# Kernel optimization log

Hardware: AMD Instinct MI355X
Metric: run time of the kernel (lower is better)

Reference implementation:

```python
import jax, jax.numpy as jnp
import numpy as np

N = 6144          # active voxels / points
C = 96            # embed_channels
B = 2             # batch size
D = H = W = 32    # sparse spatial shape
K = 16            # PFAS kNN
DEPTH = 4
GRID_OPTS = np.array([[0.1, 0.1, 0.1], [0.4, 0.4, 0.4], [0.2, 0.2, 0.2]], dtype=np.float32)
BN_EPS = 1e-5


def _bn(x, g, b):
    # BatchNorm1d in training mode: batch stats over the point dim, biased var
    m = x.mean(0)
    v = jnp.var(x, axis=0)
    return (x - m) * jax.lax.rsqrt(v + BN_EPS) * g + b


def _seg_sum(x, seg):
    return jax.ops.segment_sum(x, seg, num_segments=N)


def _forward(indices, x, fp_w, fp_b, fp_g, fp_be, att_w1, att_b1, att_w2, att_b2,
             ff_w1, ff_b1, ff_g, ff_be, ff_w2, ff_b2, sa_w1, sa_b1, sa_w2, sa_b2,
             fj_w1, fj_b1, fj_g, fj_be, fj_w2, fj_b2,
             proj_w, proj_g, proj_be, lw_w, lw_g, lw_be, w_w, adp_w,
             fuse_w, fuse_g, fuse_be, conv1_w, bn1_g, bn1_be, conv2_w, bn2_g, bn2_be):
    # ---- CMPFE ----
    p = jax.nn.relu(_bn(x @ fp_w.T + fp_b, fp_g, fp_be))            # [N,9]
    cd, cl, nm = p[:, :3], p[:, 3:6], p[:, 6:9]

    def _att(f, i):
        h = jax.nn.relu(f @ att_w1[i].T + att_b1[i])
        return jax.nn.sigmoid(h @ att_w2[i].T + att_b2[i])

    enh = jnp.concatenate([cd, cl * _att(cl, 0), nm * _att(nm, 1)], axis=1)
    fu = jax.nn.relu(_bn(enh @ ff_w1.T + ff_b1, ff_g, ff_be)) @ ff_w2.T + ff_b2
    sem = jax.nn.sigmoid(jax.nn.relu(fu @ sa_w1.T + sa_b1) @ sa_w2.T + sa_b2)
    feat = fu * sem + x * (1.0 - sem)                               # new x.features

    # ---- PFAS: kNN geometry stats ----
    coord = indices[:, 1:].astype(jnp.float32)                      # [N,3]
    batch = indices[:, 0]
    sq = jnp.sum(coord * coord, axis=1)
    d2 = sq[:, None] + sq[None, :] - 2.0 * (coord @ coord.T)
    dist = jnp.sqrt(jnp.maximum(d2, 1e-12))
    same = batch[None, :] == batch[:, None]
    eye = jnp.eye(N, dtype=bool)
    dist = jnp.where(same & ~eye, dist, jnp.inf)
    neg_nd, idx = jax.lax.top_k(-dist, K)                           # K nearest
    nbr = coord[idx]                                                # [N,K,3]
    cent = nbr - nbr.mean(axis=1, keepdims=True)
    cov = jnp.einsum('nkd,nke->nde', cent, cent) / (K - 1)
    S = jnp.linalg.svd(cov, compute_uv=False)                       # [N,3] descending
    Sn = S / (S.sum(axis=1, keepdims=True) + 1e-6)
    linearity = Sn[:, 0:1] - (Sn[:, 1] + Sn[:, 2])[:, None]
    mean_dist = (-neg_nd).mean(axis=1, keepdims=True)
    density = 1.0 / (mean_dist + 1e-6)
    fl = jax.nn.relu(_bn(feat @ fj_w1.T + fj_b1, fj_g, fj_be)) @ fj_w2.T + fj_b2
    fp_ = jax.nn.softmax(fl, axis=1)
    tower = (density * 2.0 + fp_[:, 0:1]) / 3.0
    backg = (jnp.maximum(1.0 - linearity, 1.0 - density) + fp_[:, 1:2]) / 3.0
    line = (linearity * 2.0 + fp_[:, 2:3]) / 3.0
    go = jnp.asarray(GRID_OPTS)
    lg = go[2] * jnp.array([1.0, 1.0, 5.0], jnp.float32)            # last dim *5
    grid_sizes = tower * go[0] + backg * go[1] + line * lg + 1e-6   # [N,3]

    # ---- representative grids (N > 200 path) ----
    gm = grid_sizes.mean(axis=1)
    order = jnp.argsort(gm)
    reps = [grid_sizes[order[100:200]].mean(0),
            grid_sizes[order[::-1][:100]].mean(0),
            grid_sizes[order[:100]].mean(0)]

    # ---- voxel-grid clustering (torch_geometric voxel_grid + unique inverse) ----
    start = coord.min(axis=0)

    def _cluster(size):
        size = jnp.clip(size, 1e-6, None)
        c = jnp.clip(jnp.floor((coord - start) / size).astype(jnp.int64), 0, 4095)
        mx = c.max(axis=0) + 1
        ids = ((batch.astype(jnp.int64) * mx[0] + c[:, 0]) * mx[1] + c[:, 1]) * mx[2] + c[:, 2]
        _, inv = jnp.unique(ids, return_inverse=True, size=N, fill_value=0)
        return inv.reshape(-1)

    # ---- adaptive multi-branch scatter softmax aggregation ----
    branch_feats = []
    for i in range(DEPTH - 1):
        seg = _cluster(reps[i])
        cnt = jnp.maximum(_seg_sum(jnp.ones((N, 1), feat.dtype), seg), 1.0)
        pw = jax.nn.relu(_bn(feat @ lw_w[i].T, lw_g[i], lw_be[i]))
        pw = pw - (_seg_sum(pw, seg) / cnt)[seg]
        pw = pw @ w_w[i].T
        pw = jnp.exp(pw - pw.max())
        pw = pw / (_seg_sum(pw, seg)[seg] + 1e-6)
        pf = jax.nn.relu(_bn(feat @ proj_w[i].T, proj_g[i], proj_be[i])) * pw
        branch_feats.append(_seg_sum(pf, seg)[seg])
    adp = jax.nn.softmax(feat @ adp_w.T, axis=1)                    # [N,3]
    agg = jnp.einsum('nc,ncd->nd', adp, jnp.stack(branch_feats, 1))
    last = jax.nn.relu(_bn(feat @ proj_w[-1].T, proj_g[-1], proj_be[-1]))
    fused = jax.nn.relu(_bn(jnp.concatenate([last, agg], 1) @ fuse_w.T, fuse_g, fuse_be)) + feat
    res = fused

    # ---- submanifold sparse conv block (dense scatter form; inactive sites zero,
    #      outputs gathered only at active sites == SubMConv3d) ----
    bi, zi, yi, xi = indices[:, 0], indices[:, 1], indices[:, 2], indices[:, 3]

    def _subm(f, w):
        grid = jnp.zeros((B, D, H, W, C), f.dtype).at[bi, zi, yi, xi].set(f)
        o = jax.lax.conv_general_dilated(grid, w, (1, 1, 1), 'SAME',
                                         dimension_numbers=('NDHWC', 'DHWIO', 'NDHWC'))
        return o[bi, zi, yi, xi]

    f1 = jax.nn.relu(_bn(_subm(fused, conv1_w), bn1_g, bn1_be))
    f2 = _bn(_subm(f1, conv2_w), bn2_g, bn2_be)
    return jax.nn.relu(f2 + res)


def setup_inputs() -> dict:
    key = jax.random.key(0)
    ks = iter(jax.random.split(key, 64))

    def rn(*shape, s=0.05):
        return jax.random.normal(next(ks), shape, jnp.float32) * s

    # unique active voxel coordinates
    rng = np.random.default_rng(0)
    flat = rng.choice(B * D * H * W, size=N, replace=False)
    b = flat // (D * H * W)
    r = flat % (D * H * W)
    z = r // (H * W)
    y = (r % (H * W)) // W
    xw = r % W
    indices = jnp.asarray(np.stack([b, z, y, xw], 1).astype(np.int32))
    Ch = C // 2
    return {
        'x': jax.random.normal(next(ks), (N, C), jnp.float32),
        'indices': indices,
        'fp_w': rn(9, C), 'fp_b': rn(9), 'fp_g': jnp.ones(9), 'fp_be': jnp.zeros(9),
        'att_w1': rn(2, 16, 3), 'att_b1': rn(2, 16), 'att_w2': rn(2, 3, 16), 'att_b2': rn(2, 3),
        'ff_w1': rn(C, 9), 'ff_b1': rn(C), 'ff_g': jnp.ones(C), 'ff_be': jnp.zeros(C),
        'ff_w2': rn(C, C), 'ff_b2': rn(C),
        'sa_w1': rn(Ch, C), 'sa_b1': rn(Ch), 'sa_w2': rn(1, Ch), 'sa_b2': rn(1),
        'fj_w1': rn(64, C), 'fj_b1': rn(64), 'fj_g': jnp.ones(64), 'fj_be': jnp.zeros(64),
        'fj_w2': rn(3, 64), 'fj_b2': rn(3),
        'proj_w': rn(DEPTH, C, C), 'proj_g': jnp.ones((DEPTH, C)), 'proj_be': jnp.zeros((DEPTH, C)),
        'lw_w': rn(DEPTH - 1, C, C), 'lw_g': jnp.ones((DEPTH - 1, C)), 'lw_be': jnp.zeros((DEPTH - 1, C)),
        'w_w': rn(DEPTH - 1, C, C),
        'adp_w': rn(DEPTH - 1, C),
        'fuse_w': rn(C, 2 * C), 'fuse_g': jnp.ones(C), 'fuse_be': jnp.zeros(C),
        'conv1_w': rn(3, 3, 3, C, C), 'bn1_g': jnp.ones(C), 'bn1_be': jnp.zeros(C),
        'conv2_w': rn(3, 3, 3, C, C), 'bn2_g': jnp.ones(C), 'bn2_be': jnp.zeros(C),
    }


def reference(x, indices, fp_w, fp_b, fp_g, fp_be, att_w1, att_b1, att_w2, att_b2,
              ff_w1, ff_b1, ff_g, ff_be, ff_w2, ff_b2, sa_w1, sa_b1, sa_w2, sa_b2,
              fj_w1, fj_b1, fj_g, fj_be, fj_w2, fj_b2,
              proj_w, proj_g, proj_be, lw_w, lw_g, lw_be, w_w, adp_w,
              fuse_w, fuse_g, fuse_be, conv1_w, bn1_g, bn1_be, conv2_w, bn2_g, bn2_be):
    return _forward(indices, x, fp_w, fp_b, fp_g, fp_be, att_w1, att_b1, att_w2, att_b2,
                    ff_w1, ff_b1, ff_g, ff_be, ff_w2, ff_b2, sa_w1, sa_b1, sa_w2, sa_b2,
                    fj_w1, fj_b1, fj_g, fj_be, fj_w2, fj_b2,
                    proj_w, proj_g, proj_be, lw_w, lw_g, lw_be, w_w, adp_w,
                    fuse_w, fuse_g, fuse_be, conv1_w, bn1_g, bn1_be, conv2_w, bn2_g, bn2_be)
```

## Files before the change

### kernel.cpp

```cpp
#include <hip/hip_runtime.h>
#include <cstdint>

#define NPTS 6144
#define CH 96
#define NCELEM (NPTS*CH)
#define HTSZ 16384

__device__ __forceinline__ unsigned fenc(float f){
  unsigned u = __float_as_uint(f);
  return (u & 0x80000000u) ? ~u : (u | 0x80000000u);
}
__device__ __forceinline__ float fdec(unsigned u){
  unsigned b = (u & 0x80000000u) ? (u & 0x7FFFFFFFu) : ~u;
  return __uint_as_float(b);
}

__device__ void eig3(double a00,double a01,double a02,double a11,double a12,double a22,
                     double &e0,double &e1,double &e2){
  double p1 = a01*a01 + a02*a02 + a12*a12;
  double q = (a00+a11+a22)/3.0;
  double b00=a00-q, b11=a11-q, b22=a22-q;
  double p2 = b00*b00 + b11*b11 + b22*b22 + 2.0*p1;
  if (p2 <= 1e-300){ e0=e1=e2=q; return; }
  double pp = sqrt(p2/6.0);
  double inv = 1.0/pp;
  double c00=b00*inv, c01=a01*inv, c02=a02*inv, c11=b11*inv, c12=a12*inv, c22=b22*inv;
  double det = c00*(c11*c22-c12*c12) - c01*(c01*c22-c12*c02) + c02*(c01*c12-c11*c02);
  double r = det*0.5;
  r = r < -1.0 ? -1.0 : (r > 1.0 ? 1.0 : r);
  double phi = acos(r)/3.0;
  e0 = q + 2.0*pp*cos(phi);
  e2 = q + 2.0*pp*cos(phi + 2.0943951023931953);
  e1 = 3.0*q - e0 - e2;
}

__global__ void k_zero(int* p, long n){
  long i = (long)blockIdx.x*blockDim.x + threadIdx.x;
  long st = (long)gridDim.x*blockDim.x;
  for (; i < n; i += st) p[i] = 0;
}
__global__ void k_init(int* table, int* startmin){
  int i = blockIdx.x*blockDim.x + threadIdx.x;
  if (i < 2*32*32*32) table[i] = -1;
  if (i < 3) startmin[i] = 0x7fffffff;
}
__global__ void k_htinit(unsigned long long* keys, int* vals){
  int i = blockIdx.x*blockDim.x + threadIdx.x;
  if (i < 3*HTSZ){ keys[i] = ~0ull; vals[i] = 0x7fffffff; }
}
__global__ void k_pack_min(const int* __restrict__ ind, unsigned* __restrict__ packed, int* startmin){
  __shared__ int mn[3];
  if (threadIdx.x < 3) mn[threadIdx.x] = 0x7fffffff;
  __syncthreads();
  int p = blockIdx.x*blockDim.x + threadIdx.x;
  if (p < NPTS){
    int b = ind[p*4], z = ind[p*4+1], y = ind[p*4+2], x = ind[p*4+3];
    packed[p] = (unsigned)((b<<15)|(z<<10)|(y<<5)|x);
    atomicMin(&mn[0], z); atomicMin(&mn[1], y); atomicMin(&mn[2], x);
  }
  __syncthreads();
  if (threadIdx.x < 3) atomicMin(&startmin[threadIdx.x], mn[threadIdx.x]);
}

__global__ void __launch_bounds__(256) k_mm(
    const float* __restrict__ Abase, const float* __restrict__ Wbase,
    const float* __restrict__ biasBase, float* __restrict__ Obase,
    int CIN, int COUT,
    long sA, long sW, long sO, long sBias,
    const float* __restrict__ statsBase, long sStats,
    const float* __restrict__ gBase, const float* __restrict__ beBase, long sGB,
    const float* __restrict__ SsumBase, const int* __restrict__ segBase, const int* __restrict__ cntBase,
    unsigned* maxenc, int mode)
{
  int zb = blockIdx.y;
  const float* A = Abase + (long)zb*sA;
  const float* W = Wbase + (long)zb*sW;
  float* O = Obase + (long)zb*sO;
  const float* st = statsBase ? statsBase + (long)zb*sStats : nullptr;
  const float* g  = gBase ? gBase + (long)zb*sGB : nullptr;
  const float* be = beBase ? beBase + (long)zb*sGB : nullptr;
  const float* Ss = SsumBase ? SsumBase + (long)zb*NCELEM : nullptr;
  const int* seg  = segBase ? segBase + (long)zb*NPTS : nullptr;
  const int* cnt  = cntBase ? cntBase + (long)zb*NPTS : nullptr;

  __shared__ float Al[32*97];
  __shared__ float Wl[96*97];
  int tid = threadIdx.x;
  int r0 = blockIdx.x*32;
  for (int idx = tid; idx < CIN*COUT; idx += 256){
    int co = idx / CIN, k = idx - co*CIN;
    Wl[k*97 + co] = W[idx];
  }
  for (int idx = tid; idx < 32*CIN; idx += 256){
    int ir = idx / CIN, k = idx - ir*CIN;
    int row = r0 + ir;
    float v = A[(long)row*CIN + k];
    if (mode >= 1) v = fmaxf((v - st[k*2])*st[k*2+1]*g[k] + be[k], 0.f);
    if (mode == 2){
      int s = seg[row];
      float cf = fmaxf((float)cnt[s], 1.f);
      v -= Ss[(long)s*CH + k] / cf;
    }
    Al[ir*97 + k] = v;
  }
  __syncthreads();
  float lmax = -3.4e38f;
  if (COUT == 96){
    int rp = tid >> 4, cg = tid & 15;
    int co0 = cg*6;
    float acc0[6], acc1[6];
    #pragma unroll
    for (int j=0;j<6;++j){
      float b = biasBase ? biasBase[(long)zb*sBias + co0 + j] : 0.f;
      acc0[j] = b; acc1[j] = b;
    }
    int ra = 2*rp, rb = ra+1;
    for (int k=0;k<CIN;++k){
      float a0 = Al[ra*97+k], a1 = Al[rb*97+k];
      #pragma unroll
      for (int j=0;j<6;++j){
        float w = Wl[k*97+co0+j];
        acc0[j] = fmaf(a0, w, acc0[j]);
        acc1[j] = fmaf(a1, w, acc1[j]);
      }
    }
    #pragma unroll
    for (int j=0;j<6;++j){
      O[(long)(r0+ra)*96 + co0 + j] = acc0[j];
      O[(long)(r0+rb)*96 + co0 + j] = acc1[j];
      lmax = fmaxf(lmax, fmaxf(acc0[j], acc1[j]));
    }
  } else {
    for (int idx = tid; idx < 32*COUT; idx += 256){
      int ir = idx/COUT, co = idx - ir*COUT;
      float acc = biasBase ? biasBase[(long)zb*sBias + co] : 0.f;
      for (int k=0;k<CIN;++k) acc = fmaf(Al[ir*97+k], Wl[k*97+co], acc);
      O[(long)(r0+ir)*COUT + co] = acc;
      lmax = fmaxf(lmax, acc);
    }
  }
  if (maxenc){
    __shared__ float rmx[256];
    rmx[tid] = lmax; __syncthreads();
    for (int s2=128; s2>0; s2>>=1){
      if (tid < s2) rmx[tid] = fmaxf(rmx[tid], rmx[tid+s2]);
      __syncthreads();
    }
    if (tid == 0) atomicMax(&maxenc[zb], fenc(rmx[0]));
  }
}

__global__ void __launch_bounds__(256) k_mm_fuse(
    const float* __restrict__ tp3, const float* __restrict__ st,
    const float* __restrict__ pg3, const float* __restrict__ pbe3,
    const float* __restrict__ agg, const float* __restrict__ fw, float* __restrict__ tf)
{
  __shared__ float Al[32*193];
  __shared__ float Wl[96*97];
  int tid = threadIdx.x, r0 = blockIdx.x*32;
  for (int idx = tid; idx < 32*192; idx += 256){
    int ir = idx/192, k = idx - ir*192;
    int row = r0 + ir;
    float v;
    if (k < 96){
      v = tp3[(long)row*96 + k];
      v = fmaxf((v - st[k*2])*st[k*2+1]*pg3[k] + pbe3[k], 0.f);
    } else {
      v = agg[(long)row*96 + (k-96)];
    }
    Al[ir*193 + k] = v;
  }
  int rp = tid >> 4, cg = tid & 15, co0 = cg*6;
  float acc0[6] = {0,0,0,0,0,0}, acc1[6] = {0,0,0,0,0,0};
  int ra = 2*rp, rb = ra+1;
  for (int h=0; h<2; ++h){
    __syncthreads();
    for (int idx = tid; idx < 96*96; idx += 256){
      int co = idx/96, k = idx - co*96;
      Wl[k*97+co] = fw[(long)co*192 + h*96 + k];
    }
    __syncthreads();
    for (int k=0;k<96;++k){
      float a0 = Al[ra*193 + h*96 + k], a1 = Al[rb*193 + h*96 + k];
      #pragma unroll
      for (int j=0;j<6;++j){
        float w = Wl[k*97+co0+j];
        acc0[j] = fmaf(a0, w, acc0[j]);
        acc1[j] = fmaf(a1, w, acc1[j]);
      }
    }
  }
  #pragma unroll
  for (int j=0;j<6;++j){
    tf[(long)(r0+ra)*96 + co0 + j] = acc0[j];
    tf[(long)(r0+rb)*96 + co0 + j] = acc1[j];
  }
}

__global__ void k_stats(const float* __restrict__ Abase, long sA, int COLS,
                        float* __restrict__ statsBase, long sStats){
  int col = blockIdx.x, zb = blockIdx.y;
  const float* A = Abase + (long)zb*sA;
  double s = 0.0, q = 0.0;
  for (int r = threadIdx.x; r < NPTS; r += 256){
    double v = (double)A[(long)r*COLS + col];
    s += v; q += v*v;
  }
  __shared__ double ls[256], lq[256];
  ls[threadIdx.x] = s; lq[threadIdx.x] = q; __syncthreads();
  for (int t=128; t>0; t>>=1){
    if (threadIdx.x < t){ ls[threadIdx.x] += ls[threadIdx.x+t]; lq[threadIdx.x] += lq[threadIdx.x+t]; }
    __syncthreads();
  }
  if (threadIdx.x == 0){
    double mean = ls[0]/NPTS;
    double var = lq[0]/NPTS - mean*mean;
    float* stp = statsBase + (long)zb*sStats + col*2;
    stp[0] = (float)mean;
    stp[1] = (float)(1.0/sqrt(var + 1e-5));
  }
}

__global__ void k_p_att_enh(const float* __restrict__ t9, const float* __restrict__ st,
                            const float* __restrict__ fg, const float* __restrict__ fbe,
                            const float* __restrict__ aw1, const float* __restrict__ ab1,
                            const float* __restrict__ aw2, const float* __restrict__ ab2,
                            float* __restrict__ enh){
  int p = blockIdx.x*blockDim.x + threadIdx.x;
  if (p >= NPTS) return;
  float pp[9];
  #pragma unroll
  for (int c=0;c<9;++c){
    float v = t9[p*9+c];
    pp[c] = fmaxf((v - st[c*2])*st[c*2+1]*fg[c] + fbe[c], 0.f);
  }
  float eo[9];
  eo[0]=pp[0]; eo[1]=pp[1]; eo[2]=pp[2];
  #pragma unroll
  for (int i=0;i<2;++i){
    const float* w1 = aw1 + i*48;
    const float* b1 = ab1 + i*16;
    const float* w2 = aw2 + i*48;
    const float* b2 = ab2 + i*3;
    const float* f = pp + 3 + i*3;
    float h[16];
    #pragma unroll
    for (int j=0;j<16;++j){
      float s = b1[j];
      #pragma unroll
      for (int k=0;k<3;++k) s = fmaf(f[k], w1[j*3+k], s);
      h[j] = fmaxf(s, 0.f);
    }
    #pragma unroll
    for (int o=0;o<3;++o){
      float s = b2[o];
      #pragma unroll
      for (int j=0;j<16;++j) s = fmaf(h[j], w2[o*16+j], s);
      float a = 1.f/(1.f + expf(-s));
      eo[3+i*3+o] = f[o]*a;
    }
  }
  #pragma unroll
  for (int c=0;c<9;++c) enh[p*9+c] = eo[c];
}

__global__ void __launch_bounds__(256) k_sem_feat(
    const float* __restrict__ fu, const float* __restrict__ x,
    const float* __restrict__ w1, const float* __restrict__ b1,
    const float* __restrict__ w2, const float* __restrict__ b2,
    float* __restrict__ feat){
  int wid = (blockIdx.x*blockDim.x + threadIdx.x) >> 6;
  int lane = threadIdx.x & 63;
  if (wid >= NPTS) return;
  const float* fr = fu + (long)wid*96;
  float partial = 0.f;
  if (lane < 48){
    float h = b1[lane];
    for (int k=0;k<96;++k) h = fmaf(fr[k], w1[lane*96+k], h);
    h = fmaxf(h, 0.f);
    partial = h * w2[lane];
  }
  for (int m=32; m; m>>=1) partial += __shfl_xor(partial, m);
  float sem = 1.f/(1.f + expf(-(partial + b2[0])));
  for (int c=lane; c<96; c+=64){
    float f = fr[c];
    feat[(long)wid*96+c] = f*sem + x[(long)wid*96+c]*(1.f - sem);
  }
}

__global__ void __launch_bounds__(256) k_knn(const unsigned* __restrict__ packed,
                                             const int* __restrict__ table,
                                             float* __restrict__ density, float* __restrict__ linearity){
  __shared__ unsigned pk[NPTS];
  for (int i=threadIdx.x; i<NPTS; i+=256) pk[i] = packed[i];
  __syncthreads();
  int pid = blockIdx.x*4 + (threadIdx.x>>6);
  int lane = threadIdx.x & 63;
  unsigned mypc = pk[pid];
  int myb = (int)(mypc>>15);
  int mz = (int)((mypc>>10)&31), my_=(int)((mypc>>5)&31), mx_=(int)(mypc&31);
  unsigned s[16];
  #pragma unroll
  for (int t=0;t<16;++t) s[t] = 0xFFFFFFFFu;
  int cnt = 0;
  const int tbase = myb*32768;
  for (int it=0; it<21; ++it){
    int i = lane + it*64;
    if (i < 1331){
      int dz = i/121;
      int rm = i - dz*121;
      int dy = rm/11;
      int dx = rm - dy*11;
      dz -= 5; dy -= 5; dx -= 5;
      int d2 = dz*dz + dy*dy + dx*dx;
      int zz = mz+dz, yy = my_+dy, xx = mx_+dx;
      if (d2 > 0 && d2 <= 25 &&
          (unsigned)zz < 32u && (unsigned)yy < 32u && (unsigned)xx < 32u){
        int j = table[tbase + (zz*32+yy)*32+xx];
        if (j >= 0){
          ++cnt;
          unsigned key = ((unsigned)d2<<13) | (unsigned)j;
          if (key < s[15]){
            s[15] = key;
            #pragma unroll
            for (int t=15;t>0;--t){
              unsigned a = s[t-1], b = s[t];
              unsigned lo = a<b?a:b, hi = a<b?b:a;
              s[t-1]=lo; s[t]=hi;
            }
          }
        }
      }
    }
  }
  for (int m=32; m; m>>=1) cnt += __shfl_xor(cnt, m);
  if (cnt < 16){
    #pragma unroll
    for (int t=0;t<16;++t) s[t] = 0xFFFFFFFFu;
    for (int it=0; it<96; ++it){
      int j = lane + it*64;
      unsigned pc = pk[j];
      if (j != pid && (int)(pc>>15) == myb){
        int dz = (int)((pc>>10)&31) - mz;
        int dy = (int)((pc>>5)&31) - my_;
        int dx = (int)(pc&31) - mx_;
        unsigned d2 = (unsigned)(dz*dz + dy*dy + dx*dx);
        unsigned key = (d2<<13) | (unsigned)j;
        if (key < s[15]){
          s[15] = key;
          #pragma unroll
          for (int t=15;t>0;--t){
            unsigned a = s[t-1], b = s[t];
            unsigned lo = a<b?a:b, hi = a<b?b:a;
            s[t-1]=lo; s[t]=hi;
          }
        }
      }
    }
  }
  float sdist = 0.f;
  int sz=0,sy=0,sx=0,szz=0,syy=0,sxx=0,szy=0,szx=0,syx=0;
  for (int r=0;r<16;++r){
    unsigned m = s[0];
    #pragma unroll
    for (int w=32; w; w>>=1){
      unsigned o = (unsigned)__shfl_xor((int)m, w);
      m = m<o ? m : o;
    }
    bool own = (s[0] == m);
    #pragma unroll
    for (int t=0;t<15;++t) s[t] = own ? s[t+1] : s[t];
    if (own) s[15] = 0xFFFFFFFFu;
    unsigned idx = m & 8191u;
    unsigned d2 = m >> 13;
    sdist += sqrtf((float)d2);
    unsigned pc = pk[idx];
    int nz=(int)((pc>>10)&31), ny=(int)((pc>>5)&31), nx=(int)(pc&31);
    sz+=nz; sy+=ny; sx+=nx;
    szz+=nz*nz; syy+=ny*ny; sxx+=nx*nx; szy+=nz*ny; szx+=nz*nx; syx+=ny*nx;
  }
  if (lane == 0){
    double m0 = sz/16.0, m1 = sy/16.0, m2 = sx/16.0;
    float c00 = (float)(((double)szz - 16.0*m0*m0)/15.0);
    float c11 = (float)(((double)syy - 16.0*m1*m1)/15.0);
    float c22 = (float)(((double)sxx - 16.0*m2*m2)/15.0);
    float c01 = (float)(((double)szy - 16.0*m0*m1)/15.0);
    float c02 = (float)(((double)szx - 16.0*m0*m2)/15.0);
    float c12 = (float)(((double)syx - 16.0*m1*m2)/15.0);
    double e0,e1,e2;
    eig3((double)c00,(double)c01,(double)c02,(double)c11,(double)c12,(double)c22, e0,e1,e2);
    float s0 = (float)fabs(e0), s1 = (float)fabs(e1), s2 = (float)fabs(e2);
    float den = s0 + s1 + s2 + 1e-6f;
    float sn0 = s0/den, sn1 = s1/den, sn2 = s2/den;
    linearity[pid] = sn0 - (sn1 + sn2);
    float md = sdist * (1.f/16.f);
    density[pid] = 1.f/(md + 1e-6f);
  }
}

__global__ void k_geo(const float* __restrict__ t64, const float* __restrict__ st,
                      const float* __restrict__ fg, const float* __restrict__ fbe,
                      const float* __restrict__ w2, const float* __restrict__ b2,
                      const float* __restrict__ density, const float* __restrict__ linearity,
                      float* __restrict__ gsz, float* __restrict__ gm){
  int p = blockIdx.x*blockDim.x + threadIdx.x;
  if (p >= NPTS) return;
  float fl[3];
  #pragma unroll
  for (int o=0;o<3;++o) fl[o] = b2[o];
  for (int k=0;k<64;++k){
    float v = t64[(long)p*64+k];
    v = fmaxf((v - st[k*2])*st[k*2+1]*fg[k] + fbe[k], 0.f);
    #pragma unroll
    for (int o=0;o<3;++o) fl[o] = fmaf(v, w2[o*64+k], fl[o]);
  }
  float mx = fmaxf(fl[0], fmaxf(fl[1], fl[2]));
  float e0 = expf(fl[0]-mx), e1 = expf(fl[1]-mx), e2 = expf(fl[2]-mx);
  float es = e0+e1+e2;
  float p0 = e0/es, p1 = e1/es, p2 = e2/es;
  float den = density[p], lin = linearity[p];
  float tw = (den*2.f + p0)/3.f;
  float bg = (fmaxf(1.f-lin, 1.f-den) + p1)/3.f;
  float ln = (lin*2.f + p2)/3.f;
  float g0 = tw*0.1f + bg*0.4f + ln*0.2f + 1e-6f;
  float g1 = tw*0.1f + bg*0.4f + ln*0.2f + 1e-6f;
  float g2 = tw*0.1f + bg*0.4f + ln*1.0f + 1e-6f;
  gsz[p*3+0]=g0; gsz[p*3+1]=g1; gsz[p*3+2]=g2;
  gm[p] = (g0+g1+g2)/3.f;
}

#define RNKCHUNK 768
__global__ void __launch_bounds__(256) k_rank(const float* __restrict__ gm, int* __restrict__ rank){
  __shared__ unsigned long long lk[RNKCHUNK];
  int j0 = blockIdx.y*RNKCHUNK;
  for (int i=threadIdx.x; i<RNKCHUNK; i+=256){
    int j = j0 + i;
    lk[i] = (((unsigned long long)fenc(gm[j]))<<13) | (unsigned long long)j;
  }
  __syncthreads();
  int p = blockIdx.x*256 + threadIdx.x;
  unsigned long long myk = (((unsigned long long)fenc(gm[p]))<<13) | (unsigned long long)p;
  int cnt = 0;
  #pragma unroll 4
  for (int i=0; i<RNKCHUNK; ++i) cnt += (lk[i] < myk) ? 1 : 0;
  atomicAdd(&rank[p], cnt);
}
__global__ void k_scatter(const int* __restrict__ rank, const float* __restrict__ gsz,
                          float* __restrict__ bkt){
  int p = blockIdx.x*blockDim.x + threadIdx.x;
  if (p >= NPTS) return;
  int r = rank[p];
  int z = -1, t = 0;
  if (r < 100){ z = 2; t = r; }
  else if (r < 200){ z = 0; t = r - 100; }
  else if (r >= NPTS-100){ z = 1; t = r - (NPTS-100); }
  if (z >= 0){
    #pragma unroll
    for (int d=0; d<3; ++d) bkt[(z*100 + t)*3 + d] = gsz[p*3+d];
  }
}
__global__ void k_reps(const float* __restrict__ bkt, float* __restrict__ reps){
  int i = threadIdx.x;
  if (i >= 9) return;
  int z = i/3, d = i - z*3;
  double s = 0.0;
  for (int t=0; t<100; ++t) s += (double)bkt[(z*100 + t)*3 + d];
  reps[i] = (float)(s/100.0);
}

__global__ void k_cluster_c(const int* __restrict__ ind, const float* __restrict__ reps,
                            const int* __restrict__ startmin, int* __restrict__ cbuf, int* mxbuf){
  int z = blockIdx.y;
  int p = blockIdx.x*blockDim.x + threadIdx.x;
  __shared__ int lmx[3];
  if (threadIdx.x < 3) lmx[threadIdx.x] = 0;
  __syncthreads();
  if (p < NPTS){
    #pragma unroll
    for (int d=0; d<3; ++d){
      float sizev = fmaxf(reps[z*3+d], 1e-6f);
      float cf = floorf(((float)ind[p*4+1+d] - (float)startmin[d]) / sizev);
      int ci = (int)cf;
      ci = ci < 0 ? 0 : (ci > 4095 ? 4095 : ci);
      cbuf[((long)z*NPTS + p)*3 + d] = ci;
      atomicMax(&lmx[d], ci);
    }
  }
  __syncthreads();
  if (threadIdx.x < 3) atomicMax(&mxbuf[z*3+threadIdx.x], lmx[threadIdx.x]);
// ... 223 lines not shown
}
__global__ void __launch_bounds__(256) k_conv_sum(const int* __restrict__ nbrtab,
                                                  const float* __restrict__ part,
                                                  float* __restrict__ out){
  int idx = blockIdx.x*256 + threadIdx.x;
  int p = idx/24, c4 = idx - p*24;
  const int* nt = nbrtab + p*27;
  float4 acc = make_float4(0.f,0.f,0.f,0.f);
  for (int tap=0; tap<27; ++tap){
    if (nt[tap] >= 0){
      float4 v = ((const float4*)part)[((long)p*27 + tap)*24 + c4];
      acc.x += v.x; acc.y += v.y; acc.z += v.z; acc.w += v.w;
    }
  }
  ((float4*)out)[idx] = acc;
}
__global__ void __launch_bounds__(256) k_conv_gemm_atomic(
    const float* __restrict__ src, const float* __restrict__ Wc,
    const int* __restrict__ tapcnt, const int* __restrict__ ptlist,
    float* __restrict__ out){
  int tap = blockIdx.y;
  int n = tapcnt[tap];
  int r0 = blockIdx.x*32;
  if (r0 >= n) return;
  __shared__ float Al[32*97];
  __shared__ float Wl[96*97];
  __shared__ int pqs[32];
  int tid = threadIdx.x;
  if (tid < 32){
    int r = r0 + tid;
    pqs[tid] = (r < n) ? ptlist[tap*NPTS + r] : -1;
  }
  __syncthreads();
  for (int idx4 = tid; idx4 < 2304; idx4 += 256){
    int ci = idx4/24, c4 = idx4 - ci*24;
    float4 w = ((const float4*)(Wc + ((long)tap*96 + ci)*96))[c4];
    float* d = &Wl[ci*97 + c4*4];
    d[0]=w.x; d[1]=w.y; d[2]=w.z; d[3]=w.w;
  }
  for (int idx4 = tid; idx4 < 32*24; idx4 += 256){
    int ir = idx4/24, c4 = idx4 - ir*24;
    int pq = pqs[ir];
    float4 s = make_float4(0.f,0.f,0.f,0.f);
    if (pq >= 0){
      int q = pq & 0xFFFF;
      s = ((const float4*)(src + (long)q*CH))[c4];
    }
    float* d = &Al[ir*97 + c4*4];
    d[0]=s.x; d[1]=s.y; d[2]=s.z; d[3]=s.w;
  }
  __syncthreads();
  int rp = tid >> 4, cg = tid & 15;
  int co0 = cg*6;
  int ra = 2*rp, rb = ra+1;
  float acc0[6]={0,0,0,0,0,0}, acc1[6]={0,0,0,0,0,0};
  for (int k=0;k<96;++k){
    float a0 = Al[ra*97+k], a1 = Al[rb*97+k];
    #pragma unroll
    for (int j=0;j<6;++j){
      float w = Wl[k*97+co0+j];
      acc0[j] = fmaf(a0, w, acc0[j]);
      acc1[j] = fmaf(a1, w, acc1[j]);
    }
  }
  int pa = pqs[ra], pb = pqs[rb];
  if (pa >= 0){
    float* o = out + (long)(pa>>16)*CH + co0;
    #pragma unroll
    for (int j=0;j<6;++j) atomicAdd(&o[j], acc0[j]);
  }
  if (pb >= 0){
    float* o = out + (long)(pb>>16)*CH + co0;
    #pragma unroll
    for (int j=0;j<6;++j) atomicAdd(&o[j], acc1[j]);
  }
}
__global__ void k_bnrelu(const float* __restrict__ a, const float* __restrict__ st,
                         const float* __restrict__ g, const float* __restrict__ be,
                         float* __restrict__ o){
  int idx = blockIdx.x*blockDim.x + threadIdx.x;
  int c = idx % CH;
  float v = a[idx];
  o[idx] = fmaxf((v - st[c*2])*st[c*2+1]*g[c] + be[c], 0.f);
}
__global__ void k_final(const float* __restrict__ c2, const float* __restrict__ st,
                        const float* __restrict__ g, const float* __restrict__ be,
                        const float* __restrict__ fused, float* __restrict__ out){
  int idx = blockIdx.x*blockDim.x + threadIdx.x;
  int c = idx % CH;
  float v = c2[idx];
  v = (v - st[c*2])*st[c*2+1]*g[c] + be[c];
  out[idx] = fmaxf(v + fused[idx], 0.f);
}

extern "C" void kernel_launch(void* const* d_in, const int* in_sizes, int n_in,
                              void* d_out, int out_size, void* d_ws, size_t ws_size,
                              hipStream_t stream)
{
  const float* x      = (const float*)d_in[0];
  const int*   ind    = (const int*)  d_in[1];
  const float* fp_w   = (const float*)d_in[2];
  const float* fp_b   = (const float*)d_in[3];
  const float* fp_g   = (const float*)d_in[4];
  const float* fp_be  = (const float*)d_in[5];
  const float* att_w1 = (const float*)d_in[6];
  const float* att_b1 = (const float*)d_in[7];
  const float* att_w2 = (const float*)d_in[8];
  const float* att_b2 = (const float*)d_in[9];
  const float* ff_w1  = (const float*)d_in[10];
  const float* ff_b1  = (const float*)d_in[11];
  const float* ff_g   = (const float*)d_in[12];
  const float* ff_be  = (const float*)d_in[13];
  const float* ff_w2  = (const float*)d_in[14];
  const float* ff_b2  = (const float*)d_in[15];
  const float* sa_w1  = (const float*)d_in[16];
  const float* sa_b1  = (const float*)d_in[17];
  const float* sa_w2  = (const float*)d_in[18];
  const float* sa_b2  = (const float*)d_in[19];
  const float* fj_w1  = (const float*)d_in[20];
  const float* fj_b1  = (const float*)d_in[21];
  const float* fj_g   = (const float*)d_in[22];
  const float* fj_be  = (const float*)d_in[23];
  const float* fj_w2  = (const float*)d_in[24];
  const float* fj_b2  = (const float*)d_in[25];
  const float* proj_w = (const float*)d_in[26];
  const float* proj_g = (const float*)d_in[27];
  const float* proj_be= (const float*)d_in[28];
  const float* lw_w   = (const float*)d_in[29];
  const float* lw_g   = (const float*)d_in[30];
  const float* lw_be  = (const float*)d_in[31];
  const float* w_w    = (const float*)d_in[32];
  const float* adp_w  = (const float*)d_in[33];
  const float* fuse_w = (const float*)d_in[34];
  const float* fuse_g = (const float*)d_in[35];
  const float* fuse_be= (const float*)d_in[36];
  const float* conv1_w= (const float*)d_in[37];
  const float* bn1_g  = (const float*)d_in[38];
  const float* bn1_be = (const float*)d_in[39];
  const float* conv2_w= (const float*)d_in[40];
  const float* bn2_g  = (const float*)d_in[41];
  const float* bn2_be = (const float*)d_in[42];
  float* outp = (float*)d_out;
  (void)in_sizes; (void)n_in; (void)out_size;

  char* ws = (char*)d_ws;
  size_t off = 0;
  auto alloc = [&](size_t bytes)->size_t{
    off = (off + 255) & ~(size_t)255;
    size_t o = off; off += bytes; return o;
  };
  const size_t FNC = (size_t)NCELEM*4;
  size_t o_packed = alloc((size_t)NPTS*4);
  size_t o_start  = alloc(16);
  size_t o_dens   = alloc((size_t)NPTS*4);
  size_t o_lin    = alloc((size_t)NPTS*4);
  size_t o_t9     = alloc((size_t)NPTS*9*4);
  size_t o_enh    = alloc((size_t)NPTS*9*4);
  size_t o_gm     = alloc((size_t)NPTS*4);
  size_t o_gsz    = alloc((size_t)NPTS*3*4);
  size_t o_reps   = alloc(16*4);
  size_t o_bkt    = alloc((size_t)3*100*3*4);
  size_t o_cbuf   = alloc((size_t)3*NPTS*3*4);
  size_t o_ids    = alloc((size_t)3*NPTS*8);
  size_t o_seg    = alloc((size_t)3*NPTS*4);
  size_t o_adp    = alloc((size_t)NPTS*3*4);
  size_t o_table  = alloc((size_t)65536*4);
  size_t o_nbr    = alloc((size_t)NPTS*27*4);
  size_t o_ptlist = alloc((size_t)27*NPTS*4);
  size_t o_t64    = alloc((size_t)NPTS*64*4);
  size_t o_stats  = alloc((size_t)13*192*4);
  size_t o_htk    = alloc((size_t)3*HTSZ*8);
  size_t o_htv    = alloc((size_t)3*HTSZ*4);
  size_t o_S      = alloc(3*FNC);
  size_t o_E      = alloc(3*FNC);
  size_t o_F      = alloc(3*FNC);
  size_t o_cnt    = alloc((size_t)3*NPTS*4);
  size_t o_rank   = alloc((size_t)NPTS*4);
  size_t o_tapcnt = alloc(32*4);
  size_t o_mx     = alloc(16*4);
  size_t o_maxenc = alloc(16*4);
  size_t zend = off;
  size_t o_T96 = alloc(FNC);
  size_t o_fu  = alloc(FNC);
  size_t o_feat= alloc(FNC);
  size_t o_tlw = alloc(3*FNC);
  size_t o_pw2 = alloc(3*FNC);
  size_t o_tp  = alloc(4*FNC);
  size_t o_agg = alloc(FNC);
  size_t o_tf  = alloc(FNC);
  size_t o_fsd = alloc(FNC);
  size_t o_c1  = alloc(FNC);
  size_t o_f1  = alloc(FNC);
  size_t o_c2  = alloc(FNC);
  size_t need_base = off;
  size_t o_part = alloc((size_t)NPTS*27*CH*4);
  bool use_part = (off <= ws_size);
  (void)need_base;

  float* stats = (float*)(ws + o_stats);
  long zcount = (long)((zend - o_S)/4);

  k_zero<<<dim3(2048), dim3(256), 0, stream>>>((int*)(ws+o_S), zcount);
  k_init<<<dim3(256), dim3(256), 0, stream>>>((int*)(ws+o_table), (int*)(ws+o_start));
  k_htinit<<<dim3((3*HTSZ+255)/256), dim3(256), 0, stream>>>((unsigned long long*)(ws+o_htk), (int*)(ws+o_htv));
  k_pack_min<<<dim3(24), dim3(256), 0, stream>>>(ind, (unsigned*)(ws+o_packed), (int*)(ws+o_start));
  k_table<<<dim3(24), 256, 0, stream>>>(ind, (int*)(ws+o_table));

  k_mm<<<dim3(192,1), 256, 0, stream>>>(x, fp_w, fp_b, (float*)(ws+o_t9), 96, 9,
      0,0,0,0, nullptr,0, nullptr,nullptr,0, nullptr,nullptr,nullptr, nullptr, 0);
  k_stats<<<dim3(9,1), 256, 0, stream>>>((float*)(ws+o_t9), 0, 9, stats+0*192, 0);
  k_p_att_enh<<<dim3(24), 256, 0, stream>>>((float*)(ws+o_t9), stats+0*192, fp_g, fp_be,
      att_w1, att_b1, att_w2, att_b2, (float*)(ws+o_enh));

  k_mm<<<dim3(192,1), 256, 0, stream>>>((float*)(ws+o_enh), ff_w1, ff_b1, (float*)(ws+o_T96), 9, 96,
      0,0,0,0, nullptr,0, nullptr,nullptr,0, nullptr,nullptr,nullptr, nullptr, 0);
  k_stats<<<dim3(96,1), 256, 0, stream>>>((float*)(ws+o_T96), 0, 96, stats+1*192, 0);
  k_mm<<<dim3(192,1), 256, 0, stream>>>((float*)(ws+o_T96), ff_w2, ff_b2, (float*)(ws+o_fu), 96, 96,
      0,0,0,0, stats+1*192,0, ff_g, ff_be,0, nullptr,nullptr,nullptr, nullptr, 1);

  k_sem_feat<<<dim3(1536), 256, 0, stream>>>((float*)(ws+o_fu), x, sa_w1, sa_b1, sa_w2, sa_b2,
      (float*)(ws+o_feat));

  k_knn<<<dim3(1536), 256, 0, stream>>>((unsigned*)(ws+o_packed), (int*)(ws+o_table),
      (float*)(ws+o_dens), (float*)(ws+o_lin));

  k_mm<<<dim3(192,1), 256, 0, stream>>>((float*)(ws+o_feat), fj_w1, fj_b1, (float*)(ws+o_t64), 96, 64,
      0,0,0,0, nullptr,0, nullptr,nullptr,0, nullptr,nullptr,nullptr, nullptr, 0);
  k_stats<<<dim3(64,1), 256, 0, stream>>>((float*)(ws+o_t64), 0, 64, stats+2*192, 0);
  k_geo<<<dim3(24), 256, 0, stream>>>((float*)(ws+o_t64), stats+2*192, fj_g, fj_be, fj_w2, fj_b2,
      (float*)(ws+o_dens), (float*)(ws+o_lin), (float*)(ws+o_gsz), (float*)(ws+o_gm));

  k_rank<<<dim3(24,8), 256, 0, stream>>>((float*)(ws+o_gm), (int*)(ws+o_rank));
  k_scatter<<<dim3(24), 256, 0, stream>>>((int*)(ws+o_rank), (float*)(ws+o_gsz), (float*)(ws+o_bkt));
  k_reps<<<dim3(1), 64, 0, stream>>>((float*)(ws+o_bkt), (float*)(ws+o_reps));

  k_cluster_c<<<dim3(24,3), 256, 0, stream>>>(ind, (float*)(ws+o_reps), (int*)(ws+o_start),
      (int*)(ws+o_cbuf), (int*)(ws+o_mx));
  k_cluster_ids<<<dim3(24,3), 256, 0, stream>>>(ind, (int*)(ws+o_cbuf), (int*)(ws+o_mx),
      (long long*)(ws+o_ids));
  k_seg_build<<<dim3(24,3), 256, 0, stream>>>((long long*)(ws+o_ids),
      (unsigned long long*)(ws+o_htk), (int*)(ws+o_htv));
  k_seg_lookup<<<dim3(24,3), 256, 0, stream>>>((long long*)(ws+o_ids),
      (unsigned long long*)(ws+o_htk), (int*)(ws+o_htv), (int*)(ws+o_seg), (int*)(ws+o_cnt));

  k_mm<<<dim3(192,3), 256, 0, stream>>>((float*)(ws+o_feat), lw_w, nullptr, (float*)(ws+o_tlw), 96, 96,
      0, 96*96, NCELEM, 0, nullptr,0, nullptr,nullptr,0, nullptr,nullptr,nullptr, nullptr, 0);
  k_stats<<<dim3(96,3), 256, 0, stream>>>((float*)(ws+o_tlw), NCELEM, 96, stats+3*192, 192);
  k_pw_accum<<<dim3(2304,3), 256, 0, stream>>>((float*)(ws+o_tlw), stats+3*192, lw_g, lw_be,
      (int*)(ws+o_seg), (float*)(ws+o_S));
  k_mm<<<dim3(192,3), 256, 0, stream>>>((float*)(ws+o_tlw), w_w, nullptr, (float*)(ws+o_pw2), 96, 96,
      NCELEM, 96*96, NCELEM, 0, stats+3*192,192, lw_g, lw_be,96,
      (float*)(ws+o_S), (int*)(ws+o_seg), (int*)(ws+o_cnt), (unsigned*)(ws+o_maxenc), 2);
  k_exp_accum<<<dim3(2304,3), 256, 0, stream>>>((float*)(ws+o_pw2), (unsigned*)(ws+o_maxenc),
      (int*)(ws+o_seg), (float*)(ws+o_E));
  k_mm<<<dim3(192,4), 256, 0, stream>>>((float*)(ws+o_feat), proj_w, nullptr, (float*)(ws+o_tp), 96, 96,
      0, 96*96, NCELEM, 0, nullptr,0, nullptr,nullptr,0, nullptr,nullptr,nullptr, nullptr, 0);
  k_stats<<<dim3(96,4), 256, 0, stream>>>((float*)(ws+o_tp), NCELEM, 96, stats+6*192, 192);
  k_pf_accum<<<dim3(2304,3), 256, 0, stream>>>((float*)(ws+o_tp), stats+6*192, proj_g, proj_be,
      (float*)(ws+o_pw2), (unsigned*)(ws+o_maxenc), (int*)(ws+o_seg), (float*)(ws+o_E), (float*)(ws+o_F));
  k_adp<<<dim3(24), 256, 0, stream>>>((float*)(ws+o_feat), adp_w, (float*)(ws+o_adp));
  k_agg<<<dim3(2304), 256, 0, stream>>>((float*)(ws+o_adp), (float*)(ws+o_F), (int*)(ws+o_seg),
      (float*)(ws+o_agg));

  k_mm_fuse<<<dim3(192), 256, 0, stream>>>((float*)(ws+o_tp) + (size_t)3*NCELEM, stats+9*192,
      proj_g + 3*96, proj_be + 3*96, (float*)(ws+o_agg), fuse_w, (float*)(ws+o_tf));
  k_stats<<<dim3(96,1), 256, 0, stream>>>((float*)(ws+o_tf), 0, 96, stats+10*192, 0);
  k_fused<<<dim3(2304), 256, 0, stream>>>((float*)(ws+o_tf), stats+10*192, fuse_g, fuse_be,
      (float*)(ws+o_feat), (float*)(ws+o_fsd));

  k_nbr<<<dim3((NPTS*27+255)/256), 256, 0, stream>>>(ind, (int*)(ws+o_table), (int*)(ws+o_nbr));
  k_convlist<<<dim3(24), 256, 0, stream>>>((int*)(ws+o_nbr), (int*)(ws+o_tapcnt),
      (int*)(ws+o_ptlist));
  if (use_part){
    k_conv_gemm<<<dim3(192,27), 256, 0, stream>>>((float*)(ws+o_fsd), conv1_w,
        (int*)(ws+o_tapcnt), (int*)(ws+o_ptlist), (float*)(ws+o_part));
    k_conv_sum<<<dim3(NPTS*24/256), 256, 0, stream>>>((int*)(ws+o_nbr), (float*)(ws+o_part),
        (float*)(ws+o_c1));
  } else {
    k_zero<<<dim3(2304), dim3(256), 0, stream>>>((int*)(ws+o_c1), NCELEM);
    k_conv_gemm_atomic<<<dim3(192,27), 256, 0, stream>>>((float*)(ws+o_fsd), conv1_w,
        (int*)(ws+o_tapcnt), (int*)(ws+o_ptlist), (float*)(ws+o_c1));
  }
  k_stats<<<dim3(96,1), 256, 0, stream>>>((float*)(ws+o_c1), 0, 96, stats+11*192, 0);
  k_bnrelu<<<dim3(2304), 256, 0, stream>>>((float*)(ws+o_c1), stats+11*192, bn1_g, bn1_be, (float*)(ws+o_f1));
  if (use_part){
    k_conv_gemm<<<dim3(192,27), 256, 0, stream>>>((float*)(ws+o_f1), conv2_w,
        (int*)(ws+o_tapcnt), (int*)(ws+o_ptlist), (float*)(ws+o_part));
    k_conv_sum<<<dim3(NPTS*24/256), 256, 0, stream>>>((int*)(ws+o_nbr), (float*)(ws+o_part),
        (float*)(ws+o_c2));
  } else {
    k_zero<<<dim3(2304), dim3(256), 0, stream>>>((int*)(ws+o_c2), NCELEM);
    k_conv_gemm_atomic<<<dim3(192,27), 256, 0, stream>>>((float*)(ws+o_f1), conv2_w,
        (int*)(ws+o_tapcnt), (int*)(ws+o_ptlist), (float*)(ws+o_c2));
  }
  k_stats<<<dim3(96,1), 256, 0, stream>>>((float*)(ws+o_c2), 0, 96, stats+12*192, 0);
  k_final<<<dim3(2304), 256, 0, stream>>>((float*)(ws+o_c2), stats+12*192, bn2_g, bn2_be,
      (float*)(ws+o_fsd), outp);
}
```

Before: 506.4 us.

## Sort kNN ball offsets by distance with early exit; split BN stats reduction

New measurement: 559.1 us. 1.1x slower.

```diff
diff --git a/kernel.cpp b/kernel.cpp
--- a/kernel.cpp
+++ b/kernel.cpp
@@ -5,6 +5,7 @@
 #define CH 96
 #define NCELEM (NPTS*CH)
 #define HTSZ 16384
+#define NBALL 514
 
 __device__ __forceinline__ unsigned fenc(float f){
   unsigned u = __float_as_uint(f);
@@ -60,6 +61,33 @@
   }
   __syncthreads();
   if (threadIdx.x < 3) atomicMin(&startmin[threadIdx.x], mn[threadIdx.x]);
+}
+__global__ void k_ball(unsigned* __restrict__ ball){
+  __shared__ int hcnt[32], hbase[32], hpos[32];
+  int tid = threadIdx.x;
+  if (tid < 32){ hcnt[tid] = 0; hpos[tid] = 0; }
+  __syncthreads();
+  for (int i=tid; i<1331; i+=256){
+    int dz = i/121, rm = i - dz*121, dy = rm/11, dx = rm - dy*11;
+    int a = dz-5, b = dy-5, c = dx-5;
+    int d2 = a*a + b*b + c*c;
+    if (d2 > 0 && d2 <= 25) atomicAdd(&hcnt[d2], 1);
+  }
+  __syncthreads();
+  if (tid == 0){
+    int acc = 0;
+    for (int d=1; d<=25; ++d){ hbase[d] = acc; acc += hcnt[d]; }
+  }
+  __syncthreads();
+  for (int i=tid; i<1331; i+=256){
+    int dz = i/121, rm = i - dz*121, dy = rm/11, dx = rm - dy*11;
+    int a = dz-5, b = dy-5, c = dx-5;
+    int d2 = a*a + b*b + c*c;
+    if (d2 > 0 && d2 <= 25){
+      int pos = hbase[d2] + atomicAdd(&hpos[d2], 1);
+      ball[pos] = ((unsigned)d2<<16)|((unsigned)dz<<10)|((unsigned)dy<<5)|(unsigned)dx;
+    }
+  }
 }
 
 __global__ void __launch_bounds__(256) k_mm(
@@ -197,28 +225,43 @@
   }
 }
 
-__global__ void k_stats(const float* __restrict__ Abase, long sA, int COLS,
-                        float* __restrict__ statsBase, long sStats){
-  int col = blockIdx.x, zb = blockIdx.y;
+__global__ void k_stats2(const float* __restrict__ Abase, long sA, int COLS, int RPT,
+                         double* __restrict__ part){
+  int zb = blockIdx.y, slab = blockIdx.x;
   const float* A = Abase + (long)zb*sA;
+  int tid = threadIdx.x;
+  int col = tid % COLS, ro = tid / COLS;
+  __shared__ double ls[384], lq[384];
   double s = 0.0, q = 0.0;
-  for (int r = threadIdx.x; r < NPTS; r += 256){
-    double v = (double)A[(long)r*COLS + col];
+  int rbase = slab*256;
+  for (int r = ro; r < 256; r += RPT){
+    double v = (double)A[(long)(rbase + r)*COLS + col];
     s += v; q += v*v;
   }
-  __shared__ double ls[256], lq[256];
-  ls[threadIdx.x] = s; lq[threadIdx.x] = q; __syncthreads();
-  for (int t=128; t>0; t>>=1){
-    if (threadIdx.x < t){ ls[threadIdx.x] += ls[threadIdx.x+t]; lq[threadIdx.x] += lq[threadIdx.x+t]; }
-    __syncthreads();
-  }
-  if (threadIdx.x == 0){
-    double mean = ls[0]/NPTS;
-    double var = lq[0]/NPTS - mean*mean;
-    float* stp = statsBase + (long)zb*sStats + col*2;
-    stp[0] = (float)mean;
-    stp[1] = (float)(1.0/sqrt(var + 1e-5));
-  }
+  ls[tid] = s; lq[tid] = q;
+  __syncthreads();
+  if (ro == 0){
+    for (int k=1; k<RPT; ++k){ s += ls[col + k*COLS]; q += lq[col + k*COLS]; }
+    double* o = part + (((long)zb*24 + slab)*COLS + col)*2;
+    o[0] = s; o[1] = q;
+  }
+}
+__global__ void k_stats_fin(const double* __restrict__ part, int COLS,
+                            float* __restrict__ statsBase, long sStats){
+  int col = blockIdx.x*64 + threadIdx.x;
+  int zb = blockIdx.y;
+  if (col >= COLS) return;
+  double s = 0.0, q = 0.0;
+  const double* pb = part + ((long)zb*24)*COLS*2;
+  for (int sl=0; sl<24; ++sl){
+    s += pb[((long)sl*COLS + col)*2];
+    q += pb[((long)sl*COLS + col)*2 + 1];
+  }
+  double mean = s/NPTS;
+  double var = q/NPTS - mean*mean;
+  float* stp = statsBase + (long)zb*sStats + col*2;
+  stp[0] = (float)mean;
+  stp[1] = (float)(1.0/sqrt(var + 1e-5));
 }
 
 __global__ void k_p_att_enh(const float* __restrict__ t9, const float* __restrict__ st,
@@ -290,6 +333,7 @@
 
 __global__ void __launch_bounds__(256) k_knn(const unsigned* __restrict__ packed,
                                              const int* __restrict__ table,
+                                             const unsigned* __restrict__ ball,
                                              float* __restrict__ density, float* __restrict__ linearity){
   __shared__ unsigned pk[NPTS];
   for (int i=threadIdx.x; i<NPTS; i+=256) pk[i] = packed[i];
@@ -304,18 +348,16 @@
   for (int t=0;t<16;++t) s[t] = 0xFFFFFFFFu;
   int cnt = 0;
   const int tbase = myb*32768;
-  for (int it=0; it<21; ++it){
+  for (int it=0; it<9; ++it){
     int i = lane + it*64;
-    if (i < 1331){
-      int dz = i/121;
-      int rm = i - dz*121;
-      int dy = rm/11;
-      int dx = rm - dy*11;
-      dz -= 5; dy -= 5; dx -= 5;
-      int d2 = dz*dz + dy*dy + dx*dx;
+    if (i < NBALL){
+      unsigned e = ball[i];
+      int d2 = (int)(e >> 16);
+      int dz = (int)((e>>10)&31) - 5;
+      int dy = (int)((e>>5)&31) - 5;
+      int dx = (int)(e&31) - 5;
       int zz = mz+dz, yy = my_+dy, xx = mx_+dx;
-      if (d2 > 0 && d2 <= 25 &&
-          (unsigned)zz < 32u && (unsigned)yy < 32u && (unsigned)xx < 32u){
+      if ((unsigned)zz < 32u && (unsigned)yy < 32u && (unsigned)xx < 32u){
         int j = table[tbase + (zz*32+yy)*32+xx];
         if (j >= 0){
           ++cnt;
@@ -332,9 +374,17 @@
         }
       }
     }
-  }
-  for (int m=32; m; m>>=1) cnt += __shfl_xor(cnt, m);
-  if (cnt < 16){
+    int nxt = (it+1)*64;
+    if (nxt >= NBALL) break;
+    int tot = cnt;
+    for (int m=32; m; m>>=1) tot += __shfl_xor(tot, m);
+    unsigned dlast = ball[nxt-1] >> 16;
+    unsigned dnext = ball[nxt] >> 16;
+    if (tot >= 16 && dnext > dlast) break;
+  }
+  int tot = cnt;
+  for (int m=32; m; m>>=1) tot += __shfl_xor(tot, m);
+  if (tot < 16){
     #pragma unroll
     for (int t=0;t<16;++t) s[t] = 0xFFFFFFFFu;
     for (int it=0; it<96; ++it){
@@ -864,6 +914,7 @@
   const size_t FNC = (size_t)NCELEM*4;
   size_t o_packed = alloc((size_t)NPTS*4);
   size_t o_start  = alloc(16);
+  size_t o_ball   = alloc((size_t)NBALL*4);
   size_t o_dens   = alloc((size_t)NPTS*4);
   size_t o_lin    = alloc((size_t)NPTS*4);
   size_t o_t9     = alloc((size_t)NPTS*9*4);
@@ -881,6 +932,7 @@
   size_t o_ptlist = alloc((size_t)27*NPTS*4);
   size_t o_t64    = alloc((size_t)NPTS*64*4);
   size_t o_stats  = alloc((size_t)13*192*4);
+  size_t o_spart  = alloc((size_t)4*24*96*2*8);
   size_t o_htk    = alloc((size_t)3*HTSZ*8);
   size_t o_htv    = alloc((size_t)3*HTSZ*4);
   size_t o_S      = alloc(3*FNC);
@@ -904,12 +956,11 @@
   size_t o_c1  = alloc(FNC);
   size_t o_f1  = alloc(FNC);
   size_t o_c2  = alloc(FNC);
-  size_t need_base = off;
   size_t o_part = alloc((size_t)NPTS*27*CH*4);
   bool use_part = (off <= ws_size);
-  (void)need_base;
 
   float* stats = (float*)(ws + o_stats);
+  double* spart = (double*)(ws + o_spart);
   long zcount = (long)((zend - o_S)/4);
 
   k_zero<<<dim3(2048), dim3(256), 0, stream>>>((int*)(ws+o_S), zcount);
@@ -917,16 +968,19 @@
   k_htinit<<<dim3((3*HTSZ+255)/256), dim3(256), 0, stream>>>((unsigned long long*)(ws+o_htk), (int*)(ws+o_htv));
   k_pack_min<<<dim3(24), dim3(256), 0, stream>>>(ind, (unsigned*)(ws+o_packed), (int*)(ws+o_start));
   k_table<<<dim3(24), 256, 0, stream>>>(ind, (int*)(ws+o_table));
+  k_ball<<<dim3(1), 256, 0, stream>>>((unsigned*)(ws+o_ball));
 
   k_mm<<<dim3(192,1), 256, 0, stream>>>(x, fp_w, fp_b, (float*)(ws+o_t9), 96, 9,
       0,0,0,0, nullptr,0, nullptr,nullptr,0, nullptr,nullptr,nullptr, nullptr, 0);
-  k_stats<<<dim3(9,1), 256, 0, stream>>>((float*)(ws+o_t9), 0, 9, stats+0*192, 0);
+  k_stats2<<<dim3(24,1), 252, 0, stream>>>((float*)(ws+o_t9), 0, 9, 28, spart);
+  k_stats_fin<<<dim3(1,1), 64, 0, stream>>>(spart, 9, stats+0*192, 0);
   k_p_att_enh<<<dim3(24), 256, 0, stream>>>((float*)(ws+o_t9), stats+0*192, fp_g, fp_be,
       att_w1, att_b1, att_w2, att_b2, (float*)(ws+o_enh));
 
   k_mm<<<dim3(192,1), 256, 0, stream>>>((float*)(ws+o_enh), ff_w1, ff_b1, (float*)(ws+o_T96), 9, 96,
       0,0,0,0, nullptr,0, nullptr,nullptr,0, nullptr,nullptr,nullptr, nullptr, 0);
-  k_stats<<<dim3(96,1), 256, 0, stream>>>((float*)(ws+o_T96), 0, 96, stats+1*192, 0);
+  k_stats2<<<dim3(24,1), 384, 0, stream>>>((float*)(ws+o_T96), 0, 96, 4, spart);
+  k_stats_fin<<<dim3(2,1), 64, 0, stream>>>(spart, 96, stats+1*192, 0);
   k_mm<<<dim3(192,1), 256, 0, stream>>>((float*)(ws+o_T96), ff_w2, ff_b2, (float*)(ws+o_fu), 96, 96,
       0,0,0,0, stats+1*192,0, ff_g, ff_be,0, nullptr,nullptr,nullptr, nullptr, 1);
 
@@ -934,11 +988,12 @@
       (float*)(ws+o_feat));
 
   k_knn<<<dim3(1536), 256, 0, stream>>>((unsigned*)(ws+o_packed), (int*)(ws+o_table),
-      (float*)(ws+o_dens), (float*)(ws+o_lin));
+      (unsigned*)(ws+o_ball), (float*)(ws+o_dens), (float*)(ws+o_lin));
 
   k_mm<<<dim3(192,1), 256, 0, stream>>>((float*)(ws+o_feat), fj_w1, fj_b1, (float*)(ws+o_t64), 96, 64,
       0,0,0,0, nullptr,0, nullptr,nullptr,0, nullptr,nullptr,nullptr, nullptr, 0);
-  k_stats<<<dim3(64,1), 256, 0, stream>>>((float*)(ws+o_t64), 0, 64, stats+2*192, 0);
+  k_stats2<<<dim3(24,1), 256, 0, stream>>>((float*)(ws+o_t64), 0, 64, 4, spart);
+  k_stats_fin<<<dim3(1,1), 64, 0, stream>>>(spart, 64, stats+2*192, 0);
   k_geo<<<dim3(24), 256, 0, stream>>>((float*)(ws+o_t64), stats+2*192, fj_g, fj_be, fj_w2, fj_b2,
       (float*)(ws+o_dens), (float*)(ws+o_lin), (float*)(ws+o_gsz), (float*)(ws+o_gm));
 
@@ -957,7 +1012,8 @@
 
   k_mm<<<dim3(192,3), 256, 0, stream>>>((float*)(ws+o_feat), lw_w, nullptr, (float*)(ws+o_tlw), 96, 96,
       0, 96*96, NCELEM, 0, nullptr,0, nullptr,nullptr,0, nullptr,nullptr,nullptr, nullptr, 0);
-  k_stats<<<dim3(96,3), 256, 0, stream>>>((float*)(ws+o_tlw), NCELEM, 96, stats+3*192, 192);
+  k_stats2<<<dim3(24,3), 384, 0, stream>>>((float*)(ws+o_tlw), NCELEM, 96, 4, spart);
+  k_stats_fin<<<dim3(2,3), 64, 0, stream>>>(spart, 96, stats+3*192, 192);
   k_pw_accum<<<dim3(2304,3), 256, 0, stream>>>((float*)(ws+o_tlw), stats+3*192, lw_g, lw_be,
       (int*)(ws+o_seg), (float*)(ws+o_S));
   k_mm<<<dim3(192,3), 256, 0, stream>>>((float*)(ws+o_tlw), w_w, nullptr, (float*)(ws+o_pw2), 96, 96,
@@ -967,7 +1023,8 @@
       (int*)(ws+o_seg), (float*)(ws+o_E));
   k_mm<<<dim3(192,4), 256, 0, stream>>>((float*)(ws+o_feat), proj_w, nullptr, (float*)(ws+o_tp), 96, 96,
       0, 96*96, NCELEM, 0, nullptr,0, nullptr,nullptr,0, nullptr,nullptr,nullptr, nullptr, 0);
-  k_stats<<<dim3(96,4), 256, 0, stream>>>((float*)(ws+o_tp), NCELEM, 96, stats+6*192, 192);
+  k_stats2<<<dim3(24,4), 384, 0, stream>>>((float*)(ws+o_tp), NCELEM, 96, 4, spart);
+  k_stats_fin<<<dim3(2,4), 64, 0, stream>>>(spart, 96, stats+6*192, 192);
   k_pf_accum<<<dim3(2304,3), 256, 0, stream>>>((float*)(ws+o_tp), stats+6*192, proj_g, proj_be,
       (float*)(ws+o_pw2), (unsigned*)(ws+o_maxenc), (int*)(ws+o_seg), (float*)(ws+o_E), (float*)(ws+o_F));
   k_adp<<<dim3(24), 256, 0, stream>>>((float*)(ws+o_feat), adp_w, (float*)(ws+o_adp));
@@ -976,7 +1033,8 @@
 
   k_mm_fuse<<<dim3(192), 256, 0, stream>>>((float*)(ws+o_tp) + (size_t)3*NCELEM, stats+9*192,
       proj_g + 3*96, proj_be + 3*96, (float*)(ws+o_agg), fuse_w, (float*)(ws+o_tf));
-  k_stats<<<dim3(96,1), 256, 0, stream>>>((float*)(ws+o_tf), 0, 96, stats+10*192, 0);
+  k_stats2<<<dim3(24,1), 384, 0, stream>>>((float*)(ws+o_tf), 0, 96, 4, spart);
+  k_stats_fin<<<dim3(2,1), 64, 0, stream>>>(spart, 96, stats+10*192, 0);
   k_fused<<<dim3(2304), 256, 0, stream>>>((float*)(ws+o_tf), stats+10*192, fuse_g, fuse_be,
       (float*)(ws+o_feat), (float*)(ws+o_fsd));
 
@@ -993,7 +1051,8 @@
     k_conv_gemm_atomic<<<dim3(192,27), 256, 0, stream>>>((float*)(ws+o_fsd), conv1_w,
         (int*)(ws+o_tapcnt), (int*)(ws+o_ptlist), (float*)(ws+o_c1));
   }
-  k_stats<<<dim3(96,1), 256, 0, stream>>>((float*)(ws+o_c1), 0, 96, stats+11*192, 0);
+  k_stats2<<<dim3(24,1), 384, 0, stream>>>((float*)(ws+o_c1), 0, 96, 4, spart);
+  k_stats_fin<<<dim3(2,1), 64, 0, stream>>>(spart, 96, stats+11*192, 0);
   k_bnrelu<<<dim3(2304), 256, 0, stream>>>((float*)(ws+o_c1), stats+11*192, bn1_g, bn1_be, (float*)(ws+o_f1));
   if (use_part){
     k_conv_gemm<<<dim3(192,27), 256, 0, stream>>>((float*)(ws+o_f1), conv2_w,
@@ -1005,7 +1064,8 @@
     k_conv_gemm_atomic<<<dim3(192,27), 256, 0, stream>>>((float*)(ws+o_f1), conv2_w,
         (int*)(ws+o_tapcnt), (int*)(ws+o_ptlist), (float*)(ws+o_c2));
   }
-  k_stats<<<dim3(96,1), 256, 0, stream>>>((float*)(ws+o_c2), 0, 96, stats+12*192, 0);
+  k_stats2<<<dim3(24,1), 384, 0, stream>>>((float*)(ws+o_c2), 0, 96, 4, spart);
+  k_stats_fin<<<dim3(2,1), 64, 0, stream>>>(spart, 96, stats+12*192, 0);
   k_final<<<dim3(2304), 256, 0, stream>>>((float*)(ws+o_c2), stats+12*192, bn2_g, bn2_be,
       (float*)(ws+o_fsd), outp);
 }
```
